# Performance work log

Measured on AMD Instinct MI355X. Metric: run time of the kernel, lower is better.

## Reference

```python
import jax, jax.numpy as jnp
import numpy as np

N, E, F_IN, H, D = 50000, 800000, 256, 4, 128


def _gat_layer(x, W, al, ar, bias, src, dst):
    # x: [N, Fin]; W: [Fin, H*D]; al/ar: [H, D]; bias: [H*D]
    feat = (x @ W).reshape(N, H, D)                      # [N,H,D]
    el = jnp.einsum('nhd,hd->nh', feat, al)              # [N,H]
    er = jnp.einsum('nhd,hd->nh', feat, ar)              # [N,H]
    e = jax.nn.leaky_relu(el[src] + er[dst], negative_slope=0.2)  # [E,H]
    # edge softmax over incoming edges of each dst node (numerically stable)
    emax = jax.ops.segment_max(e, dst, num_segments=N)   # [N,H]
    ee = jnp.exp(e - emax[dst])                          # [E,H]
    denom = jax.ops.segment_sum(ee, dst, num_segments=N) # [N,H]
    a = ee / denom[dst]                                  # [E,H]
    # weighted scatter-aggregate of source features
    out = jax.ops.segment_sum(feat[src] * a[:, :, None], dst, num_segments=N)  # [N,H,D]
    return out + bias.reshape(H, D)


def setup_inputs() -> dict:
    key = jax.random.key(0)
    ks = jax.random.split(key, 16)
    f32 = jnp.float32
    nfeats = jax.random.normal(ks[0], (N, F_IN), dtype=f32)
    src = jax.random.randint(ks[1], (E,), 0, N, dtype=jnp.int32)
    dst = jax.random.randint(ks[2], (E,), 0, N, dtype=jnp.int32)
    def lin(k, fin):
        return jax.random.normal(k, (fin, H * D), dtype=f32) / np.sqrt(fin).astype(np.float32)
    def attn(k):
        return jax.random.normal(k, (H, D), dtype=f32) / np.sqrt(D).astype(np.float32)
    return {
        'nfeats': nfeats,
        'W1': lin(ks[3], F_IN), 'al1': attn(ks[4]), 'ar1': attn(ks[5]), 'b1': jnp.zeros((H * D,), f32),
        'W2': lin(ks[6], D),    'al2': attn(ks[7]), 'ar2': attn(ks[8]), 'b2': jnp.zeros((H * D,), f32),
        'W3': lin(ks[9], D),    'al3': attn(ks[10]), 'ar3': attn(ks[11]), 'b3': jnp.zeros((H * D,), f32),
        'Wc': jax.random.normal(ks[12], (D, 1), dtype=f32) / np.sqrt(D).astype(np.float32),
        'bc': jnp.zeros((1,), f32),
        'src': src, 'dst': dst,
    }


def reference(nfeats, W1, al1, ar1, b1, W2, al2, ar2, b2, W3, al3, ar3, b3, Wc, bc, src, dst):
    h = jnp.mean(jax.nn.relu(_gat_layer(nfeats, W1, al1, ar1, b1, src, dst)), axis=1)  # [N,D]
    h = jnp.mean(jax.nn.relu(_gat_layer(h, W2, al2, ar2, b2, src, dst)), axis=1)
    h = jnp.mean(jax.nn.relu(_gat_layer(h, W3, al3, ar3, b3, src, dst)), axis=1)
    hg = jnp.mean(h, axis=0, keepdims=True)  # readout: mean over nodes -> [1,D]
    return jax.nn.sigmoid(hg @ Wc + bc)      # [1,1]
```

## Files before the change

kernel.cpp:

```cpp
#include <hip/hip_runtime.h>
#include <hip/hip_bf16.h>

#define N_NODES 50000
#define E_EDGES 800000
#define HD 512
#define H_HEADS 4
#define D_DIM 128
#define N_PAD 53248

typedef __attribute__((ext_vector_type(8))) short bf16x8;
typedef __attribute__((ext_vector_type(4))) float f32x4;
typedef __attribute__((ext_vector_type(2))) float f32x2;

__device__ __forceinline__ unsigned short f2b(float f) {
  unsigned u = __float_as_uint(f);
  u += 0x7FFFu + ((u >> 16) & 1u);
  return (unsigned short)(u >> 16);
}
__device__ __forceinline__ float b2f(unsigned short s) {
  return __uint_as_float(((unsigned)s) << 16);
}
__device__ __forceinline__ float lrelu(float v) { return v > 0.f ? v : 0.2f * v; }
__device__ __forceinline__ float sel4(float a, float b, float c, float d, int h) {
  return h == 0 ? a : (h == 1 ? b : (h == 2 ? c : d));
}
__device__ __forceinline__ float sel4v(float4 v, int h) {
  return sel4(v.x, v.y, v.z, v.w, h);
}

#define GLOAD_LDS16(g, l)                                             \
  __builtin_amdgcn_global_load_lds(                                   \
      (const __attribute__((address_space(1))) void*)(g),             \
      (__attribute__((address_space(3))) void*)(l), 16, 0, 0)

__global__ void cast_f2b(const float* __restrict__ in, unsigned short* __restrict__ out, int n4) {
  int i = blockIdx.x * blockDim.x + threadIdx.x;
  if (i >= n4) return;
  float4 v = *(const float4*)(in + (size_t)i * 4);
  ushort4 o;
  o.x = f2b(v.x); o.y = f2b(v.y); o.z = f2b(v.z); o.w = f2b(v.w);
  *(ushort4*)(out + (size_t)i * 4) = o;
}

__global__ void transpose_cast_all(const float* __restrict__ W1, const float* __restrict__ W2,
                                   const float* __restrict__ W3,
                                   unsigned short* __restrict__ WT1,
                                   unsigned short* __restrict__ WT2,
                                   unsigned short* __restrict__ WT3) {
  int idx = blockIdx.x * blockDim.x + threadIdx.x;
  const float* W;
  unsigned short* WT;
  int K, base;
  if (idx < 131072) {
    W = W1; WT = WT1; K = 256; base = idx;
  } else if (idx < 196608) {
    W = W2; WT = WT2; K = 128; base = idx - 131072;
  } else if (idx < 262144) {
    W = W3; WT = WT3; K = 128; base = idx - 196608;
  } else {
    return;
  }
  int k = base / HD, c = base & (HD - 1);
  WT[(size_t)c * K + k] = f2b(W[(size_t)k * HD + c]);
}

__global__ __launch_bounds__(512) void gemm_mfma(const unsigned short* __restrict__ X,
                                                 const unsigned short* __restrict__ WT,
                                                 unsigned char* __restrict__ featq,
                                                 const float* __restrict__ al,
                                                 const float* __restrict__ ar,
                                                 float* __restrict__ el, float* __restrict__ er,
                                                 int K) {
  __shared__ unsigned short Atile[128 * 64];
  __shared__ unsigned short Btile[256 * 64];
  __shared__ float eds[2][2][2][128];
  const int tid = threadIdx.x;
  const int w = tid >> 6, l = tid & 63;
  const int wr = w >> 2, wc = w & 3;
  const int row0 = blockIdx.x * 128;
  const int by = blockIdx.y;
  const int col0 = by * 256;
  const int fr = l & 15;
  const int g = l >> 4;
  const int fk = g * 8;
  f32x4 acc[4][4] = {};

  for (int k0 = 0; k0 < K; k0 += 64) {
#pragma unroll
    for (int j = 0; j < 2; ++j) {
      int idx = j * 512 + tid;
      int row = idx >> 3;
      int ksw = ((idx & 7) << 3) ^ ((row & 7) << 3);
      int arow = row0 + row;
      if (arow >= N_NODES) arow = N_NODES - 1;
      GLOAD_LDS16(X + (size_t)arow * K + k0 + ksw,
                  (char*)Atile + j * 8192 + w * 1024);
    }
#pragma unroll
    for (int j = 0; j < 4; ++j) {
      int idx = j * 512 + tid;
      int row = idx >> 3;
      int ksw = ((idx & 7) << 3) ^ ((row & 7) << 3);
      GLOAD_LDS16(WT + (size_t)(col0 + row) * K + k0 + ksw,
                  (char*)Btile + j * 8192 + w * 1024);
    }
    __syncthreads();
#pragma unroll
    for (int kk = 0; kk < 64; kk += 32) {
      const int kel2 = (kk + fk) * 2;
      bf16x8 af[4], bf[4];
#pragma unroll
      for (int m = 0; m < 4; ++m) {
        int arow = wr * 64 + m * 16 + fr;
        af[m] = *(const bf16x8*)((const char*)Atile + arow * 128 + (kel2 ^ ((arow & 7) << 4)));
        int bcol = wc * 64 + m * 16 + fr;
        bf[m] = *(const bf16x8*)((const char*)Btile + bcol * 128 + (kel2 ^ ((bcol & 7) << 4)));
      }
#pragma unroll
      for (int m = 0; m < 4; ++m)
#pragma unroll
        for (int n = 0; n < 4; ++n)
          acc[m][n] = __builtin_amdgcn_mfma_f32_16x16x32_bf16(af[m], bf[n], acc[m][n], 0, 0, 0);
    }
    __syncthreads();
  }

#pragma unroll
  for (int m = 0; m < 4; ++m) {
#pragma unroll
    for (int i = 0; i < 4; ++i) {
      int r = row0 + wr * 64 + m * 16 + g * 4 + i;
      if (r < N_NODES) {
#pragma unroll
        for (int n = 0; n < 4; ++n) {
          int b = __builtin_amdgcn_cvt_pk_fp8_f32(acc[m][n][i], acc[m][n][i], 0, false);
          featq[(size_t)r * HD + col0 + wc * 64 + n * 16 + fr] = (unsigned char)(b & 0xFF);
        }
      }
    }
  }

  const int hl = wc >> 1, half = wc & 1;
  const int h = by * 2 + hl;
  float alk[4], ark[4];
#pragma unroll
  for (int n = 0; n < 4; ++n) {
    int c = h * D_DIM + half * 64 + n * 16 + fr;
    alk[n] = al[c];
    ark[n] = ar[c];
  }
#pragma unroll
  for (int m = 0; m < 4; ++m) {
#pragma unroll
    for (int i = 0; i < 4; ++i) {
      float pel = 0.f, per = 0.f;
#pragma unroll
      for (int n = 0; n < 4; ++n) {
        pel = fmaf(acc[m][n][i], alk[n], pel);
        per = fmaf(acc[m][n][i], ark[n], per);
      }
#pragma unroll
      for (int o = 1; o < 16; o <<= 1) {
        pel += __shfl_xor(pel, o);
        per += __shfl_xor(per, o);
      }
      if (fr == 0) {
        int rloc = wr * 64 + m * 16 + g * 4 + i;
        eds[0][half][hl][rloc] = pel;
        eds[1][half][hl][rloc] = per;
      }
    }
  }
  __syncthreads();
  {
    int row = tid >> 2, q = tid & 3;
    int hl2 = q & 1, sel = q >> 1;
    int r = row0 + row;
    if (r < N_NODES) {
      float v = eds[sel][0][hl2][row] + eds[sel][1][hl2][row];
      float* dst = (sel ? er : el);
      dst[(size_t)r * 4 + by * 2 + hl2] = v;
    }
  }
}

__global__ void histo_kernel(const int* __restrict__ dst, unsigned* __restrict__ deg) {
  int e = blockIdx.x * blockDim.x + threadIdx.x;
  if (e >= E_EDGES) return;
  atomicAdd(&deg[dst[e]], 1u);
}

__global__ void scan_local(const unsigned* __restrict__ deg, unsigned* __restrict__ off,
                           unsigned* __restrict__ bsum) {
  __shared__ unsigned warp_sums[16];
  const int tid = threadIdx.x;
  const int wid = tid >> 6;
  int i = blockIdx.x * 4096 + tid * 4;
  uint4 v = *(const uint4*)(deg + i);
  unsigned sm = v.x + v.y + v.z + v.w;
  unsigned x = sm;
#pragma unroll
  for (int o = 1; o < 64; o <<= 1) {
    unsigned y = __shfl_up(x, o);
    if ((tid & 63) >= o) x += y;
  }
  if ((tid & 63) == 63) warp_sums[wid] = x;
  __syncthreads();
  if (tid < 16) {
    unsigned s = warp_sums[tid];
#pragma unroll
    for (int o = 1; o < 16; o <<= 1) {
      unsigned y = __shfl_up(s, o);
      if (tid >= o) s += y;
    }
    warp_sums[tid] = s;
  }
  __syncthreads();
  unsigned wprev = (wid > 0) ? warp_sums[wid - 1] : 0u;
  unsigned ex = wprev + (x - sm);
  uint4 o4;
  o4.x = ex;
  o4.y = ex + v.x;
  o4.z = o4.y + v.y;
  o4.w = o4.z + v.z;
  *(uint4*)(off + i) = o4;
  if (tid == 1023) bsum[blockIdx.x] = warp_sums[15];
}

__global__ void scan_bsums(unsigned* __restrict__ bsum) {
  int t = threadIdx.x;
  unsigned v = (t < 13) ? bsum[t] : 0u;
  unsigned x = v;
#pragma unroll
  for (int o = 1; o < 16; o <<= 1) {
    unsigned y = __shfl_up(x, o);
    if (t >= o) x += y;
  }
  if (t < 13) bsum[t] = x - v;
}

__global__ void scan_add(unsigned* __restrict__ off, const unsigned* __restrict__ bsum,
                         unsigned* __restrict__ cursor) {
  int i = (blockIdx.x * 1024 + threadIdx.x) * 4;
  unsigned p = bsum[blockIdx.x];
  uint4 v = *(const uint4*)(off + i);
  v.x += p; v.y += p; v.z += p; v.w += p;
  *(uint4*)(off + i) = v;
  *(uint4*)(cursor + i) = v;
}

__global__ void scatter_kernel(const int* __restrict__ src, const int* __restrict__ dst,
                               unsigned* __restrict__ cursor, int* __restrict__ csr_src) {
  int e = blockIdx.x * blockDim.x + threadIdx.x;
  if (e >= E_EDGES) return;
  int d = dst[e];
  unsigned pos = atomicAdd(&cursor[d], 1u);
  csr_src[pos] = src[e];
}

__global__ __launch_bounds__(64) void agg_fused(const unsigned* __restrict__ off,
                                                const int* __restrict__ csr_src,
                                                const float* __restrict__ el,
                                                const float* __restrict__ er,
                                                const unsigned char* __restrict__ featq,
                                                const float* __restrict__ bias,
                                                unsigned short* __restrict__ hbuf) {
  __shared__ float4 ws4[64];
  const int n = blockIdx.x, t = threadIdx.x;
  const int h = t >> 4, d0 = (t & 15) * 8;
  const unsigned beg = off[n];
  const int deg = (int)(off[n + 1] - beg);
  const float NEG = -3.0e38f;
  float4 rr = *(const float4*)(er + (size_t)n * 4);
  f32x2 acc2[4] = {};

  if (deg <= 64) {
    float4 v = {NEG, NEG, NEG, NEG};
    if (t < deg) {
      int s = csr_src[beg + t];
      float4 ll = *(const float4*)(el + (size_t)s * 4);
      v.x = lrelu(ll.x + rr.x);
      v.y = lrelu(ll.y + rr.y);
      v.z = lrelu(ll.z + rr.z);
      v.w = lrelu(ll.w + rr.w);
    }
    float m0 = v.x, m1 = v.y, m2 = v.z, m3 = v.w;
#pragma unroll
    for (int o = 32; o >= 1; o >>= 1) {
      m0 = fmaxf(m0, __shfl_xor(m0, o));
      m1 = fmaxf(m1, __shfl_xor(m1, o));
      m2 = fmaxf(m2, __shfl_xor(m2, o));
      m3 = fmaxf(m3, __shfl_xor(m3, o));
    }
    float4 ev = {0.f, 0.f, 0.f, 0.f};
    if (t < deg) {
      ev.x = __expf(v.x - m0);
      ev.y = __expf(v.y - m1);
      ev.z = __expf(v.z - m2);
      ev.w = __expf(v.w - m3);
    }
    float s0 = ev.x, s1 = ev.y, s2 = ev.z, s3 = ev.w;
#pragma unroll
    for (int o = 32; o >= 1; o >>= 1) {
      s0 += __shfl_xor(s0, o);
      s1 += __shfl_xor(s1, o);
      s2 += __shfl_xor(s2, o);
      s3 += __shfl_xor(s3, o);
    }
    ws4[t] = ev;
    float invh = 1.0f / sel4(s0, s1, s2, s3, h);
    __syncthreads();
    const unsigned char* fq = featq + t * 8;
    for (int j0 = 0; j0 < deg; j0 += 4) {
      int i1 = (j0 + 1 < deg) ? j0 + 1 : j0;
      int i2 = (j0 + 2 < deg) ? j0 + 2 : j0;
      int i3 = (j0 + 3 < deg) ? j0 + 3 : j0;
      int sa = csr_src[beg + j0], sb = csr_src[beg + i1];
      int sc = csr_src[beg + i2], sd = csr_src[beg + i3];
      uint2 qa = *(const uint2*)(fq + (size_t)sa * HD);
      uint2 qb = *(const uint2*)(fq + (size_t)sb * HD);
      uint2 qc = *(const uint2*)(fq + (size_t)sc * HD);
      uint2 qd = *(const uint2*)(fq + (size_t)sd * HD);
      float wa = sel4v(ws4[j0], h) * invh;
      float wb = sel4v(ws4[i1], h) * invh;
      float wc2 = sel4v(ws4[i2], h) * invh;
      float wd = sel4v(ws4[i3], h) * invh;
      if (j0 + 1 >= deg) wb = 0.f;
      if (j0 + 2 >= deg) wc2 = 0.f;
      if (j0 + 3 >= deg) wd = 0.f;
      f32x2 w2;
      w2 = (f32x2){wa, wa};
      acc2[0] += __builtin_amdgcn_cvt_pk_f32_fp8((int)qa.x, false) * w2;
      acc2[1] += __builtin_amdgcn_cvt_pk_f32_fp8((int)qa.x, true) * w2;
      acc2[2] += __builtin_amdgcn_cvt_pk_f32_fp8((int)qa.y, false) * w2;
      acc2[3] += __builtin_amdgcn_cvt_pk_f32_fp8((int)qa.y, true) * w2;
      w2 = (f32x2){wb, wb};
      acc2[0] += __builtin_amdgcn_cvt_pk_f32_fp8((int)qb.x, false) * w2;
      acc2[1] += __builtin_amdgcn_cvt_pk_f32_fp8((int)qb.x, true) * w2;
      acc2[2] += __builtin_amdgcn_cvt_pk_f32_fp8((int)qb.y, false) * w2;
      acc2[3] += __builtin_amdgcn_cvt_pk_f32_fp8((int)qb.y, true) * w2;
      w2 = (f32x2){wc2, wc2};
      acc2[0] += __builtin_amdgcn_cvt_pk_f32_fp8((int)qc.x, false) * w2;
      acc2[1] += __builtin_amdgcn_cvt_pk_f32_fp8((int)qc.x, true) * w2;
      acc2[2] += __builtin_amdgcn_cvt_pk_f32_fp8((int)qc.y, false) * w2;
      acc2[3] += __builtin_amdgcn_cvt_pk_f32_fp8((int)qc.y, true) * w2;
      w2 = (f32x2){wd, wd};
      acc2[0] += __builtin_amdgcn_cvt_pk_f32_fp8((int)qd.x, false) * w2;
      acc2[1] += __builtin_amdgcn_cvt_pk_f32_fp8((int)qd.x, true) * w2;
      acc2[2] += __builtin_amdgcn_cvt_pk_f32_fp8((int)qd.y, false) * w2;
      acc2[3] += __builtin_amdgcn_cvt_pk_f32_fp8((int)qd.y, true) * w2;
    }
  } else {
    float m[4] = {NEG, NEG, NEG, NEG};
    for (int j = t; j < deg; j += 64) {
      int s = csr_src[beg + j];
      float4 ll = *(const float4*)(el + (size_t)s * 4);
      m[0] = fmaxf(m[0], lrelu(ll.x + rr.x));
      m[1] = fmaxf(m[1], lrelu(ll.y + rr.y));
      m[2] = fmaxf(m[2], lrelu(ll.z + rr.z));
      m[3] = fmaxf(m[3], lrelu(ll.w + rr.w));
    }
#pragma unroll
    for (int o = 32; o >= 1; o >>= 1) {
      m[0] = fmaxf(m[0], __shfl_xor(m[0], o));
      m[1] = fmaxf(m[1], __shfl_xor(m[1], o));
      m[2] = fmaxf(m[2], __shfl_xor(m[2], o));
      m[3] = fmaxf(m[3], __shfl_xor(m[3], o));
    }
    float sm[4] = {0.f, 0.f, 0.f, 0.f};
    for (int j = t; j < deg; j += 64) {
      int s = csr_src[beg + j];
      float4 ll = *(const float4*)(el + (size_t)s * 4);
      sm[0] += __expf(lrelu(ll.x + rr.x) - m[0]);
      sm[1] += __expf(lrelu(ll.y + rr.y) - m[1]);
      sm[2] += __expf(lrelu(ll.z + rr.z) - m[2]);
      sm[3] += __expf(lrelu(ll.w + rr.w) - m[3]);
    }
#pragma unroll
    for (int o = 32; o >= 1; o >>= 1) {
      sm[0] += __shfl_xor(sm[0], o);
      sm[1] += __shfl_xor(sm[1], o);
      sm[2] += __shfl_xor(sm[2], o);
      sm[3] += __shfl_xor(sm[3], o);
    }
    float mh = sel4(m[0], m[1], m[2], m[3], h);
    float ih = 1.0f / sel4(sm[0], sm[1], sm[2], sm[3], h);
    float rrh = sel4(rr.x, rr.y, rr.z, rr.w, h);
    for (int j = 0; j < deg; ++j) {
      int sj = csr_src[beg + j];
      float llh = el[(size_t)sj * 4 + h];
      float w = __expf(lrelu(llh + rrh) - mh) * ih;
      uint2 q = *(const uint2*)(featq + (size_t)sj * HD + t * 8);
      f32x2 w2 = {w, w};
      acc2[0] += __builtin_amdgcn_cvt_pk_f32_fp8((int)q.x, false) * w2;
      acc2[1] += __builtin_amdgcn_cvt_pk_f32_fp8((int)q.x, true) * w2;
      acc2[2] += __builtin_amdgcn_cvt_pk_f32_fp8((int)q.y, false) * w2;
      acc2[3] += __builtin_amdgcn_cvt_pk_f32_fp8((int)q.y, true) * w2;
    }
  }

  const float* bp = bias + h * D_DIM + d0;
  float4 b0 = *(const float4*)bp, b1 = *(const float4*)(bp + 4);
  float bv[8] = {b0.x, b0.y, b0.z, b0.w, b1.x, b1.y, b1.z, b1.w};
  float r[8];
#pragma unroll
  for (int i = 0; i < 8; ++i) r[i] = fmaxf(acc2[i >> 1][i & 1] + bv[i], 0.f);
#pragma unroll
  for (int i = 0; i < 8; ++i) {
    r[i] += __shfl_xor(r[i], 16);
    r[i] += __shfl_xor(r[i], 32);
  }
  if (h == 0) {
    uint4 o;
    o.x = (unsigned)f2b(r[0] * 0.25f) | ((unsigned)f2b(r[1] * 0.25f) << 16);
    o.y = (unsigned)f2b(r[2] * 0.25f) | ((unsigned)f2b(r[3] * 0.25f) << 16);
    o.z = (unsigned)f2b(r[4] * 0.25f) | ((unsigned)f2b(r[5] * 0.25f) << 16);
    o.w = (unsigned)f2b(r[6] * 0.25f) | ((unsigned)f2b(r[7] * 0.25f) << 16);
    *(uint4*)(hbuf + (size_t)n * D_DIM + d0) = o;
  }
}

__global__ void colsum(const unsigned short* __restrict__ hbuf, float* __restrict__ hg) {
  int d = threadIdx.x;
  float s = 0.0f;
  for (int n = blockIdx.x; n < N_NODES; n += gridDim.x)
    s += b2f(hbuf[(size_t)n * D_DIM + d]);
  atomicAdd(&hg[d], s);
}

__global__ void final_k(const float* __restrict__ hg, const float* __restrict__ Wc,
                        const float* __restrict__ bc, float* __restrict__ out) {
  int l = threadIdx.x;
  float v = hg[l] * Wc[l] + hg[l + 64] * Wc[l + 64];
#pragma unroll
  for (int off = 32; off >= 1; off >>= 1) v += __shfl_xor(v, off);
  if (l == 0) {
    float x = v * (1.0f / N_NODES) + bc[0];
    out[0] = 1.0f / (1.0f + expf(-x));
  }
}

extern "C" void kernel_launch(void* const* d_in, const int* in_sizes, int n_in,
                              void* d_out, int out_size, void* d_ws, size_t ws_size,
                              hipStream_t stream) {
  const float* nfeats = (const float*)d_in[0];
  const float* W1 = (const float*)d_in[1];
  const float* al1 = (const float*)d_in[2];
  const float* ar1 = (const float*)d_in[3];
  const float* b1 = (const float*)d_in[4];
  const float* W2 = (const float*)d_in[5];
  const float* al2 = (const float*)d_in[6];
  const float* ar2 = (const float*)d_in[7];
  const float* b2 = (const float*)d_in[8];
  const float* W3 = (const float*)d_in[9];
  const float* al3 = (const float*)d_in[10];
  const float* ar3 = (const float*)d_in[11];
  const float* b3 = (const float*)d_in[12];
  const float* Wc = (const float*)d_in[13];
  const float* bc = (const float*)d_in[14];
  const int* src = (const int*)d_in[15];
  const int* dst = (const int*)d_in[16];
  float* out = (float*)d_out;

  char* p = (char*)d_ws;
  auto carve = [&](size_t bytes) {
    char* r = p;
    p += (bytes + 255) & ~(size_t)255;
    return r;
  };
  float* el = (float*)carve((size_t)N_NODES * 4 * 4);
  float* er = (float*)carve((size_t)N_NODES * 4 * 4);
  float* hg = (float*)carve(512);
  unsigned* deg = (unsigned*)carve((size_t)N_PAD * 4);
  unsigned* offv = (unsigned*)carve((size_t)(N_PAD + 4) * 4);
  unsigned* cursor = (unsigned*)carve((size_t)N_PAD * 4);
  unsigned* bsum = (unsigned*)carve(64 * 4);
  int* csr_src = (int*)carve((size_t)E_EDGES * 4);
  unsigned char* featq = (unsigned char*)carve((size_t)N_NODES * HD);
  unsigned short* hbufb = (unsigned short*)carve((size_t)N_NODES * D_DIM * 2);
  unsigned short* xb = (unsigned short*)carve((size_t)(N_NODES + 128) * 256 * 2);
  unsigned short* WT1 = (unsigned short*)carve((size_t)HD * 256 * 2);
  unsigned short* WT2 = (unsigned short*)carve((size_t)HD * 128 * 2);
  unsigned short* WT3 = (unsigned short*)carve((size_t)HD * 128 * 2);

  hipMemsetAsync(deg, 0, (size_t)N_PAD * sizeof(unsigned), stream);
  histo_kernel<<<(E_EDGES + 255) / 256, 256, 0, stream>>>(dst, deg);
  scan_local<<<13, 1024, 0, stream>>>(deg, offv, bsum);
  scan_bsums<<<1, 64, 0, stream>>>(bsum);
  scan_add<<<13, 1024, 0, stream>>>(offv, bsum, cursor);
  scatter_kernel<<<(E_EDGES + 255) / 256, 256, 0, stream>>>(src, dst, cursor, csr_src);

  cast_f2b<<<(N_NODES * 256 / 4 + 255) / 256, 256, 0, stream>>>(nfeats, xb, N_NODES * 256 / 4);
  transpose_cast_all<<<(262144 + 255) / 256, 256, 0, stream>>>(W1, W2, W3, WT1, WT2, WT3);

  auto run_layer = [&](const unsigned short* X, int K, const unsigned short* WT,
                       const float* alv, const float* arv, const float* bv) {
    dim3 g((N_NODES + 127) / 128, 2);
    gemm_mfma<<<g, 512, 0, stream>>>(X, WT, featq, alv, arv, el, er, K);
    agg_fused<<<N_NODES, 64, 0, stream>>>(offv, csr_src, el, er, featq, bv, hbufb);
  };

  run_layer(xb, 256, WT1, al1, ar1, b1);
  run_layer(hbufb, 128, WT2, al2, ar2, b2);
  run_layer(hbufb, 128, WT3, al3, ar3, b3);

  hipMemsetAsync(hg, 0, 512, stream);
  colsum<<<1024, 128, 0, stream>>>(hbufb, hg);
  final_k<<<1, 64, 0, stream>>>(hg, Wc, bc, out);
}
```

Before: 446.0 us.

## Widen GEMM block to cover all 512 output columns with 1024 threads

The feature GEMM previously used a 2D grid, with each 512-thread block computing 256 of the 512 output columns, so every A tile was loaded twice. Each 1024-thread block now computes all 512 columns for its 128 rows. A is loaded once per block, and all four heads' el/er attention logits are produced in a single block without a second grid dimension. This doubles LDS for the B tile (64KB+) and halves the block count, which may reduce occupancy and latency hiding.

```diff
diff --git a/kernel.cpp b/kernel.cpp
--- a/kernel.cpp
+++ b/kernel.cpp
@@ -64,45 +64,42 @@
   WT[(size_t)c * K + k] = f2b(W[(size_t)k * HD + c]);
 }
 
-__global__ __launch_bounds__(512) void gemm_mfma(const unsigned short* __restrict__ X,
-                                                 const unsigned short* __restrict__ WT,
-                                                 unsigned char* __restrict__ featq,
-                                                 const float* __restrict__ al,
-                                                 const float* __restrict__ ar,
-                                                 float* __restrict__ el, float* __restrict__ er,
-                                                 int K) {
+__global__ __launch_bounds__(1024) void gemm_mfma(const unsigned short* __restrict__ X,
+                                                  const unsigned short* __restrict__ WT,
+                                                  unsigned char* __restrict__ featq,
+                                                  const float* __restrict__ al,
+                                                  const float* __restrict__ ar,
+                                                  float* __restrict__ el, float* __restrict__ er,
+                                                  int K) {
   __shared__ unsigned short Atile[128 * 64];
-  __shared__ unsigned short Btile[256 * 64];
-  __shared__ float eds[2][2][2][128];
+  __shared__ unsigned short Btile[512 * 64];
+  __shared__ float eds[2][2][4][128];
   const int tid = threadIdx.x;
   const int w = tid >> 6, l = tid & 63;
-  const int wr = w >> 2, wc = w & 3;
+  const int wr = w >> 3, wc = w & 7;
   const int row0 = blockIdx.x * 128;
-  const int by = blockIdx.y;
-  const int col0 = by * 256;
   const int fr = l & 15;
   const int g = l >> 4;
   const int fk = g * 8;
   f32x4 acc[4][4] = {};
 
   for (int k0 = 0; k0 < K; k0 += 64) {
-#pragma unroll
-    for (int j = 0; j < 2; ++j) {
-      int idx = j * 512 + tid;
+    {
+      int idx = tid;
       int row = idx >> 3;
       int ksw = ((idx & 7) << 3) ^ ((row & 7) << 3);
       int arow = row0 + row;
       if (arow >= N_NODES) arow = N_NODES - 1;
       GLOAD_LDS16(X + (size_t)arow * K + k0 + ksw,
-                  (char*)Atile + j * 8192 + w * 1024);
+                  (char*)Atile + w * 1024);
     }
 #pragma unroll
     for (int j = 0; j < 4; ++j) {
-      int idx = j * 512 + tid;
+      int idx = j * 1024 + tid;
       int row = idx >> 3;
       int ksw = ((idx & 7) << 3) ^ ((row & 7) << 3);
-      GLOAD_LDS16(WT + (size_t)(col0 + row) * K + k0 + ksw,
-                  (char*)Btile + j * 8192 + w * 1024);
+      GLOAD_LDS16(WT + (size_t)row * K + k0 + ksw,
+                  (char*)Btile + j * 16384 + w * 1024);
     }
     __syncthreads();
 #pragma unroll
@@ -134,18 +131,17 @@
 #pragma unroll
         for (int n = 0; n < 4; ++n) {
           int b = __builtin_amdgcn_cvt_pk_fp8_f32(acc[m][n][i], acc[m][n][i], 0, false);
-          featq[(size_t)r * HD + col0 + wc * 64 + n * 16 + fr] = (unsigned char)(b & 0xFF);
+          featq[(size_t)r * HD + wc * 64 + n * 16 + fr] = (unsigned char)(b & 0xFF);
         }
       }
     }
   }
 
-  const int hl = wc >> 1, half = wc & 1;
-  const int h = by * 2 + hl;
+  const int h = wc >> 1, half = wc & 1;
   float alk[4], ark[4];
 #pragma unroll
   for (int n = 0; n < 4; ++n) {
-    int c = h * D_DIM + half * 64 + n * 16 + fr;
+    int c = wc * 64 + n * 16 + fr;
     alk[n] = al[c];
     ark[n] = ar[c];
   }
@@ -166,20 +162,20 @@
       }
       if (fr == 0) {
         int rloc = wr * 64 + m * 16 + g * 4 + i;
-        eds[0][half][hl][rloc] = pel;
-        eds[1][half][hl][rloc] = per;
+        eds[0][half][h][rloc] = pel;
+        eds[1][half][h][rloc] = per;
       }
     }
   }
   __syncthreads();
   {
-    int row = tid >> 2, q = tid & 3;
-    int hl2 = q & 1, sel = q >> 1;
+    int row = tid >> 3, q = tid & 7;
+    int sel = q >> 2, hh = q & 3;
     int r = row0 + row;
     if (r < N_NODES) {
-      float v = eds[sel][0][hl2][row] + eds[sel][1][hl2][row];
+      float v = eds[sel][0][hh][row] + eds[sel][1][hh][row];
       float* dst = (sel ? er : el);
-      dst[(size_t)r * 4 + by * 2 + hl2] = v;
+      dst[(size_t)r * 4 + hh] = v;
     }
   }
 }
@@ -495,8 +491,7 @@
 
   auto run_layer = [&](const unsigned short* X, int K, const unsigned short* WT,
                        const float* alv, const float* arv, const float* bv) {
-    dim3 g((N_NODES + 127) / 128, 2);
-    gemm_mfma<<<g, 512, 0, stream>>>(X, WT, featq, alv, arv, el, er, K);
+    gemm_mfma<<<(N_NODES + 127) / 128, 1024, 0, stream>>>(X, WT, featq, alv, arv, el, er, K);
     agg_fused<<<N_NODES, 64, 0, stream>>>(offv, csr_src, el, er, featq, bv, hbufb);
   };
 
```

Measured after the change: 454.2 us. About the same (+1.8%).
